# Optimization experiments

Hardware: AMD Instinct MI355X
Metric: run time of the kernel (lower is better)

The kernel has to match this reference:

```python
import jax, jax.numpy as jnp
import numpy as np

LORA_ALPHA = 2.0

def setup_inputs() -> dict:
    key = jax.random.key(0)
    k1, k2, k3, k4 = jax.random.split(key, 4)
    B, S, D_IN, D_OUT, R = 4, 2048, 4096, 4096, 16
    x = jax.random.normal(k1, (B, S, D_IN), dtype=jnp.float32)
    weight = jax.random.normal(k2, (D_OUT, D_IN), dtype=jnp.float32) * (1.0 / np.sqrt(D_IN))
    lora_A = jax.random.normal(k3, (R, D_IN), dtype=jnp.float32) * (1.0 / np.sqrt(D_IN))
    lora_B = jax.random.normal(k4, (D_OUT, R), dtype=jnp.float32) * 0.02
    return {"x": x, "weight": weight, "lora_A": lora_A, "lora_B": lora_B}

def reference(x, weight, lora_A, lora_B):
    # main_out = F.linear(x, weight) = x @ weight.T
    main_out = jnp.einsum('bsd,od->bso', x, weight)
    # Faithful to source: materialize lora_weight = B @ A (out x in), then full linear
    lora_weight = lora_B @ lora_A  # [out, in]
    lora_out = jnp.einsum('bsd,od->bso', x, lora_weight) * LORA_ALPHA
    return main_out + lora_out
```

## Files before the change

kernel.cpp:

```cpp
#include <hip/hip_runtime.h>
#include <stdint.h>

typedef __attribute__((ext_vector_type(8))) short bf16x8;
typedef __attribute__((ext_vector_type(4))) float f32x4;

#define GM 8192
#define GN 4096
#define GK 4096
#define KTILES (GK / 64)

__device__ __forceinline__ unsigned short f2bf(float f) {
  union { float f; unsigned int u; } c; c.f = f;
  unsigned int u = c.u;
  unsigned int r = u + 0x7FFFu + ((u >> 16) & 1u);
  return (unsigned short)(r >> 16);
}

__global__ __launch_bounds__(256) void cvt_x_kernel(const float* __restrict__ x,
                                                    unsigned short* __restrict__ xb) {
  int i = blockIdx.x * 256 + threadIdx.x;
  const float4* p = (const float4*)x + (size_t)i * 2;
  float4 a = p[0], b = p[1];
  unsigned short t[8] = { f2bf(a.x), f2bf(a.y), f2bf(a.z), f2bf(a.w),
                          f2bf(b.x), f2bf(b.y), f2bf(b.z), f2bf(b.w) };
  int4 pk; __builtin_memcpy(&pk, t, 16);
  ((int4*)xb)[i] = pk;
}

__global__ __launch_bounds__(256) void weff_kernel(const float* __restrict__ w,
                                                   const float* __restrict__ lA,
                                                   const float* __restrict__ lB,
                                                   unsigned short* __restrict__ wb) {
  const int K = GK;
  int idx = blockIdx.x * 256 + threadIdx.x;
  int o  = idx >> 9;
  int i0 = (idx & 511) << 3;

  float bl[16];
#pragma unroll
  for (int r = 0; r < 16; r += 4) {
    float4 v = *(const float4*)(lB + o * 16 + r);
    bl[r] = v.x; bl[r + 1] = v.y; bl[r + 2] = v.z; bl[r + 3] = v.w;
  }

  float acc[8] = {0.f, 0.f, 0.f, 0.f, 0.f, 0.f, 0.f, 0.f};
#pragma unroll
  for (int r = 0; r < 16; ++r) {
    float4 a0 = *(const float4*)(lA + (size_t)r * K + i0);
    float4 a1 = *(const float4*)(lA + (size_t)r * K + i0 + 4);
    acc[0] += bl[r] * a0.x; acc[1] += bl[r] * a0.y;
    acc[2] += bl[r] * a0.z; acc[3] += bl[r] * a0.w;
    acc[4] += bl[r] * a1.x; acc[5] += bl[r] * a1.y;
    acc[6] += bl[r] * a1.z; acc[7] += bl[r] * a1.w;
  }

  float4 w0 = *(const float4*)(w + (size_t)o * K + i0);
  float4 w1 = *(const float4*)(w + (size_t)o * K + i0 + 4);
  unsigned short t[8] = {
    f2bf(w0.x + 2.0f * acc[0]), f2bf(w0.y + 2.0f * acc[1]),
    f2bf(w0.z + 2.0f * acc[2]), f2bf(w0.w + 2.0f * acc[3]),
    f2bf(w1.x + 2.0f * acc[4]), f2bf(w1.y + 2.0f * acc[5]),
    f2bf(w1.z + 2.0f * acc[6]), f2bf(w1.w + 2.0f * acc[7]) };
  int4 pk; __builtin_memcpy(&pk, t, 16);
  ((int4*)wb)[idx] = pk;
}


__device__ __forceinline__ void gload16(const unsigned short* g, char* l) {
  __builtin_amdgcn_global_load_lds((__attribute__((address_space(1))) void*)g,
                                   (__attribute__((address_space(3))) void*)l, 16, 0, 0);
}

__device__ __forceinline__ void barrier_fence() {
  __builtin_amdgcn_sched_barrier(0);
  asm volatile("" ::: "memory");
  __builtin_amdgcn_s_barrier();
  asm volatile("" ::: "memory");
  __builtin_amdgcn_sched_barrier(0);
}

#define MFMA_BF16(a, b, c) __builtin_amdgcn_mfma_f32_16x16x32_bf16((a), (b), (c), 0, 0, 0)

template <int HALF>
__device__ __forceinline__ void stage_half(const unsigned short* A, const unsigned short* B,
                                           char* smem, int bm0, int bn0, int w, int lane,
                                           int kt, int buf) {
  int sr, isB;
  if constexpr (HALF == 0)      { sr = w + (w & 4);                 isB = 0; }
  else if constexpr (HALF == 1) { sr = ((w >> 1) << 2) + (w & 1);   isB = 1; }
  else if constexpr (HALF == 2) { sr = ((w >> 1) << 2) + (w & 1) + 2; isB = 1; }
  else                          { sr = w + (w & 4) + 4;             isB = 0; }
  const unsigned short* mat = isB ? B : A;
  const int grow = (isB ? bn0 : bm0) + sr * 16 + (lane >> 2);
  const int gcol = ((lane & 3) * 8) ^ ((lane & 32) ? 16 : 0);
#pragma unroll
  for (int sc = 0; sc < 2; ++sc) {
    const unsigned short* src = mat + (size_t)grow * GK + kt * 64 + sc * 32 + gcol;
    char* dst = smem + (buf << 16) + (isB ? 32768 : 0) + ((sr * 2 + sc) << 10);
    gload16(src, dst);
  }
}

__device__ __forceinline__ bf16x8 ldsA(const char* smem, int buf, int sr, int sc, int foff) {
  return *(const bf16x8*)(smem + (buf << 16) + ((sr * 2 + sc) << 10) + foff);
}
__device__ __forceinline__ bf16x8 ldsB(const char* smem, int buf, int sr, int sc, int foff) {
  return *(const bf16x8*)(smem + (buf << 16) + 32768 + ((sr * 2 + sc) << 10) + foff);
}

__global__ __launch_bounds__(512, 2) void gemm_bt_kernel(const unsigned short* __restrict__ A,
                                                         const unsigned short* __restrict__ B,
                                                         float* __restrict__ C) {
  __shared__ alignas(16) char smem[131072];

  const int t = threadIdx.x, lane = t & 63, w = t >> 6;
  const int wm = w >> 2, wn = w & 3;

  const int bid = blockIdx.x;
  const int wg  = (bid & 7) * (512 / 8) + (bid >> 3);
  const int bx = wg & 15, by = wg >> 4;
  const int bm0 = by * 256, bn0 = bx * 256;

  int foff = (lane & 15) * 64 + ((lane >> 4) << 4);
  foff ^= ((foff >> 9) & 1) << 5;

  stage_half<0>(A, B, smem, bm0, bn0, w, lane, 0, 0);
  stage_half<1>(A, B, smem, bm0, bn0, w, lane, 0, 0);
  stage_half<2>(A, B, smem, bm0, bn0, w, lane, 0, 0);
  stage_half<3>(A, B, smem, bm0, bn0, w, lane, 0, 0);
  asm volatile("s_waitcnt vmcnt(0)" ::: "memory");
  barrier_fence();

  f32x4 acc[8][4] = {};
  bf16x8 av[4][2], bv0[2][2], bv1[2][2];

  for (int kt = 0; kt < KTILES; ++kt) {
    const int cur = kt & 1, nxt = cur ^ 1;
    const bool last = (kt == KTILES - 1);

#pragma unroll
    for (int mi = 0; mi < 4; ++mi) {
      av[mi][0] = ldsA(smem, cur, wm * 8 + mi, 0, foff);
      av[mi][1] = ldsA(smem, cur, wm * 8 + mi, 1, foff);
    }
#pragma unroll
    for (int ni = 0; ni < 2; ++ni) {
      bv0[ni][0] = ldsB(smem, cur, wn * 4 + ni, 0, foff);
      bv0[ni][1] = ldsB(smem, cur, wn * 4 + ni, 1, foff);
    }
    if (!last) {
      stage_half<0>(A, B, smem, bm0, bn0, w, lane, kt + 1, nxt);
      asm volatile("s_waitcnt vmcnt(4)" ::: "memory");
    } else {
      asm volatile("s_waitcnt vmcnt(2)" ::: "memory");
    }
    barrier_fence();
    __builtin_amdgcn_s_setprio(1);
#pragma unroll
    for (int mi = 0; mi < 4; ++mi)
#pragma unroll
      for (int ni = 0; ni < 2; ++ni) {
        acc[mi][ni] = MFMA_BF16(av[mi][0], bv0[ni][0], acc[mi][ni]);
        acc[mi][ni] = MFMA_BF16(av[mi][1], bv0[ni][1], acc[mi][ni]);
      }
    __builtin_amdgcn_s_setprio(0);
    barrier_fence();

#pragma unroll
    for (int ni = 0; ni < 2; ++ni) {
      bv1[ni][0] = ldsB(smem, cur, wn * 4 + 2 + ni, 0, foff);
      bv1[ni][1] = ldsB(smem, cur, wn * 4 + 2 + ni, 1, foff);
    }
    if (!last) {
      stage_half<1>(A, B, smem, bm0, bn0, w, lane, kt + 1, nxt);
      asm volatile("s_waitcnt vmcnt(4)" ::: "memory");
    } else {
      asm volatile("s_waitcnt vmcnt(0)" ::: "memory");
    }
    barrier_fence();
    __builtin_amdgcn_s_setprio(1);
#pragma unroll
    for (int mi = 0; mi < 4; ++mi)
#pragma unroll
      for (int ni = 0; ni < 2; ++ni) {
        acc[mi][2 + ni] = MFMA_BF16(av[mi][0], bv1[ni][0], acc[mi][2 + ni]);
        acc[mi][2 + ni] = MFMA_BF16(av[mi][1], bv1[ni][1], acc[mi][2 + ni]);
      }
    __builtin_amdgcn_s_setprio(0);
    barrier_fence();

#pragma unroll
    for (int mi = 0; mi < 4; ++mi) {
      av[mi][0] = ldsA(smem, cur, wm * 8 + 4 + mi, 0, foff);
      av[mi][1] = ldsA(smem, cur, wm * 8 + 4 + mi, 1, foff);
    }
    if (!last) stage_half<2>(A, B, smem, bm0, bn0, w, lane, kt + 1, nxt);
    barrier_fence();
    __builtin_amdgcn_s_setprio(1);
#pragma unroll
    for (int mi = 0; mi < 4; ++mi)
#pragma unroll
      for (int ni = 0; ni < 2; ++ni) {
        acc[4 + mi][2 + ni] = MFMA_BF16(av[mi][0], bv1[ni][0], acc[4 + mi][2 + ni]);
        acc[4 + mi][2 + ni] = MFMA_BF16(av[mi][1], bv1[ni][1], acc[4 + mi][2 + ni]);
      }
    __builtin_amdgcn_s_setprio(0);
    barrier_fence();

    if (!last) {
      stage_half<3>(A, B, smem, bm0, bn0, w, lane, kt + 1, nxt);
      asm volatile("s_waitcnt vmcnt(4)" ::: "memory");
    }
    barrier_fence();
    __builtin_amdgcn_s_setprio(1);
#pragma unroll
    for (int mi = 0; mi < 4; ++mi)
#pragma unroll
      for (int ni = 0; ni < 2; ++ni) {
        acc[4 + mi][ni] = MFMA_BF16(av[mi][0], bv0[ni][0], acc[4 + mi][ni]);
        acc[4 + mi][ni] = MFMA_BF16(av[mi][1], bv0[ni][1], acc[4 + mi][ni]);
      }
    __builtin_amdgcn_s_setprio(0);
    barrier_fence();
  }

  const int orow = (lane >> 4) << 2;
#pragma unroll
  for (int mi = 0; mi < 8; ++mi) {
#pragma unroll
    for (int ni = 0; ni < 4; ++ni) {
      float* cp = C + (size_t)(bm0 + wm * 128 + mi * 16 + orow) * GN
                    + (bn0 + wn * 64 + ni * 16 + (lane & 15));
#pragma unroll
      for (int r = 0; r < 4; ++r)
        cp[(size_t)r * GN] = acc[mi][ni][r];
    }
  }
}

extern "C" void kernel_launch(void* const* d_in, const int* in_sizes, int n_in,
                              void* d_out, int out_size, void* d_ws, size_t ws_size,
                              hipStream_t stream) {
  const float* x  = (const float*)d_in[0];
  const float* w  = (const float*)d_in[1];
  const float* lA = (const float*)d_in[2];
  const float* lB = (const float*)d_in[3];
  float* out = (float*)d_out;

  const int M = GM, N = GN, K = GK;

  unsigned short* xb = (unsigned short*)d_ws;
  unsigned short* wb = xb + (size_t)M * K;

  cvt_x_kernel<<<dim3((M * K / 8) / 256), dim3(256), 0, stream>>>(x, xb);
  weff_kernel<<<dim3((N * K / 8) / 256), dim3(256), 0, stream>>>(w, lA, lB, wb);
  gemm_bt_kernel<<<dim3((M / 256) * (N / 256)), dim3(512), 0, stream>>>(xb, wb, out);
}
```

Measured before the change: 329.2 us.

## Deepen GEMM prefetch pipeline, drop sched barriers, and tile weff over 8 rows

The GEMM main loop now issues the first quarter of the K-tile two steps ahead into the current buffer, shifting every staging call earlier by one phase. The waitcnt thresholds are adjusted so more global loads stay in flight across barriers. The sched_barrier fences are removed in favour of plain barriers plus explicit lgkmcnt waits, which gives the compiler more freedom to interleave LDS reads with MFMAs. The weff kernel now computes an 8x8 output tile per thread so lora_A loads are reused across 8 rows, at the cost of more registers and scalar lora_B loads. The deeper prefetch risks LDS races if the buffer reuse ordering is wrong.

```diff
diff --git a/kernel.cpp b/kernel.cpp
--- a/kernel.cpp
+++ b/kernel.cpp
@@ -33,36 +33,42 @@
                                                    unsigned short* __restrict__ wb) {
   const int K = GK;
   int idx = blockIdx.x * 256 + threadIdx.x;
-  int o  = idx >> 9;
-  int i0 = (idx & 511) << 3;
-
-  float bl[16];
-#pragma unroll
-  for (int r = 0; r < 16; r += 4) {
-    float4 v = *(const float4*)(lB + o * 16 + r);
-    bl[r] = v.x; bl[r + 1] = v.y; bl[r + 2] = v.z; bl[r + 3] = v.w;
-  }
-
-  float acc[8] = {0.f, 0.f, 0.f, 0.f, 0.f, 0.f, 0.f, 0.f};
+  int cg = idx & 511;
+  int rg = idx >> 9;
+  int i0 = cg << 3;
+  int o0 = rg << 3;
+
+  float acc[8][8];
+#pragma unroll
+  for (int r = 0; r < 8; ++r)
+#pragma unroll
+    for (int c = 0; c < 8; ++c) acc[r][c] = 0.f;
+
 #pragma unroll
   for (int r = 0; r < 16; ++r) {
     float4 a0 = *(const float4*)(lA + (size_t)r * K + i0);
     float4 a1 = *(const float4*)(lA + (size_t)r * K + i0 + 4);
-    acc[0] += bl[r] * a0.x; acc[1] += bl[r] * a0.y;
-    acc[2] += bl[r] * a0.z; acc[3] += bl[r] * a0.w;
-    acc[4] += bl[r] * a1.x; acc[5] += bl[r] * a1.y;
-    acc[6] += bl[r] * a1.z; acc[7] += bl[r] * a1.w;
-  }
-
-  float4 w0 = *(const float4*)(w + (size_t)o * K + i0);
-  float4 w1 = *(const float4*)(w + (size_t)o * K + i0 + 4);
-  unsigned short t[8] = {
-    f2bf(w0.x + 2.0f * acc[0]), f2bf(w0.y + 2.0f * acc[1]),
-    f2bf(w0.z + 2.0f * acc[2]), f2bf(w0.w + 2.0f * acc[3]),
-    f2bf(w1.x + 2.0f * acc[4]), f2bf(w1.y + 2.0f * acc[5]),
-    f2bf(w1.z + 2.0f * acc[6]), f2bf(w1.w + 2.0f * acc[7]) };
-  int4 pk; __builtin_memcpy(&pk, t, 16);
-  ((int4*)wb)[idx] = pk;
+    float av[8] = { a0.x, a0.y, a0.z, a0.w, a1.x, a1.y, a1.z, a1.w };
+#pragma unroll
+    for (int row = 0; row < 8; ++row) {
+      float b = lB[(size_t)(o0 + row) * 16 + r];
+#pragma unroll
+      for (int c = 0; c < 8; ++c) acc[row][c] += b * av[c];
+    }
+  }
+
+#pragma unroll
+  for (int row = 0; row < 8; ++row) {
+    float4 w0 = *(const float4*)(w + (size_t)(o0 + row) * K + i0);
+    float4 w1 = *(const float4*)(w + (size_t)(o0 + row) * K + i0 + 4);
+    unsigned short t[8] = {
+      f2bf(w0.x + 2.0f * acc[row][0]), f2bf(w0.y + 2.0f * acc[row][1]),
+      f2bf(w0.z + 2.0f * acc[row][2]), f2bf(w0.w + 2.0f * acc[row][3]),
+      f2bf(w1.x + 2.0f * acc[row][4]), f2bf(w1.y + 2.0f * acc[row][5]),
+      f2bf(w1.z + 2.0f * acc[row][6]), f2bf(w1.w + 2.0f * acc[row][7]) };
+    int4 pk; __builtin_memcpy(&pk, t, 16);
+    *(int4*)(wb + (size_t)(o0 + row) * K + i0) = pk;
+  }
 }
 
 
@@ -71,12 +77,10 @@
                                    (__attribute__((address_space(3))) void*)l, 16, 0, 0);
 }
 
-__device__ __forceinline__ void barrier_fence() {
-  __builtin_amdgcn_sched_barrier(0);
+__device__ __forceinline__ void bar() {
   asm volatile("" ::: "memory");
   __builtin_amdgcn_s_barrier();
   asm volatile("" ::: "memory");
-  __builtin_amdgcn_sched_barrier(0);
 }
 
 #define MFMA_BF16(a, b, c) __builtin_amdgcn_mfma_f32_16x16x32_bf16((a), (b), (c), 0, 0, 0)
@@ -86,10 +90,10 @@
                                            char* smem, int bm0, int bn0, int w, int lane,
                                            int kt, int buf) {
   int sr, isB;
-  if constexpr (HALF == 0)      { sr = w + (w & 4);                 isB = 0; }
-  else if constexpr (HALF == 1) { sr = ((w >> 1) << 2) + (w & 1);   isB = 1; }
+  if constexpr (HALF == 0)      { sr = w + (w & 4);                   isB = 0; }
+  else if constexpr (HALF == 1) { sr = ((w >> 1) << 2) + (w & 1);     isB = 1; }
   else if constexpr (HALF == 2) { sr = ((w >> 1) << 2) + (w & 1) + 2; isB = 1; }
-  else                          { sr = w + (w & 4) + 4;             isB = 0; }
+  else                          { sr = w + (w & 4) + 4;               isB = 0; }
   const unsigned short* mat = isB ? B : A;
   const int grow = (isB ? bn0 : bm0) + sr * 16 + (lane >> 2);
   const int gcol = ((lane & 3) * 8) ^ ((lane & 32) ? 16 : 0);
@@ -128,15 +132,17 @@
   stage_half<1>(A, B, smem, bm0, bn0, w, lane, 0, 0);
   stage_half<2>(A, B, smem, bm0, bn0, w, lane, 0, 0);
   stage_half<3>(A, B, smem, bm0, bn0, w, lane, 0, 0);
-  asm volatile("s_waitcnt vmcnt(0)" ::: "memory");
-  barrier_fence();
+  stage_half<0>(A, B, smem, bm0, bn0, w, lane, 1, 1);
+  asm volatile("s_waitcnt vmcnt(6)" ::: "memory");
+  bar();
 
   f32x4 acc[8][4] = {};
   bf16x8 av[4][2], bv0[2][2], bv1[2][2];
 
   for (int kt = 0; kt < KTILES; ++kt) {
-    const int cur = kt & 1, nxt = cur ^ 1;
-    const bool last = (kt == KTILES - 1);
+    const int cur = kt & 1;
+    const bool n1 = (kt + 1 < KTILES);
+    const bool n2 = (kt + 2 < KTILES);
 
 #pragma unroll
     for (int mi = 0; mi < 4; ++mi) {
@@ -148,13 +154,14 @@
       bv0[ni][0] = ldsB(smem, cur, wn * 4 + ni, 0, foff);
       bv0[ni][1] = ldsB(smem, cur, wn * 4 + ni, 1, foff);
     }
-    if (!last) {
-      stage_half<0>(A, B, smem, bm0, bn0, w, lane, kt + 1, nxt);
-      asm volatile("s_waitcnt vmcnt(4)" ::: "memory");
+    if (n1) {
+      stage_half<1>(A, B, smem, bm0, bn0, w, lane, kt + 1, cur ^ 1);
+      asm volatile("s_waitcnt vmcnt(6)" ::: "memory");
     } else {
       asm volatile("s_waitcnt vmcnt(2)" ::: "memory");
     }
-    barrier_fence();
+    bar();
+    asm volatile("s_waitcnt lgkmcnt(0)" ::: "memory");
     __builtin_amdgcn_s_setprio(1);
 #pragma unroll
     for (int mi = 0; mi < 4; ++mi)
@@ -164,20 +171,21 @@
         acc[mi][ni] = MFMA_BF16(av[mi][1], bv0[ni][1], acc[mi][ni]);
       }
     __builtin_amdgcn_s_setprio(0);
-    barrier_fence();
+    bar();
 
 #pragma unroll
     for (int ni = 0; ni < 2; ++ni) {
       bv1[ni][0] = ldsB(smem, cur, wn * 4 + 2 + ni, 0, foff);
       bv1[ni][1] = ldsB(smem, cur, wn * 4 + 2 + ni, 1, foff);
     }
-    if (!last) {
-      stage_half<1>(A, B, smem, bm0, bn0, w, lane, kt + 1, nxt);
-      asm volatile("s_waitcnt vmcnt(4)" ::: "memory");
+    if (n1) {
+      stage_half<2>(A, B, smem, bm0, bn0, w, lane, kt + 1, cur ^ 1);
+      asm volatile("s_waitcnt vmcnt(6)" ::: "memory");
     } else {
       asm volatile("s_waitcnt vmcnt(0)" ::: "memory");
     }
-    barrier_fence();
+    bar();
+    asm volatile("s_waitcnt lgkmcnt(0)" ::: "memory");
     __builtin_amdgcn_s_setprio(1);
 #pragma unroll
     for (int mi = 0; mi < 4; ++mi)
@@ -187,15 +195,16 @@
         acc[mi][2 + ni] = MFMA_BF16(av[mi][1], bv1[ni][1], acc[mi][2 + ni]);
       }
     __builtin_amdgcn_s_setprio(0);
-    barrier_fence();
+    bar();
 
 #pragma unroll
     for (int mi = 0; mi < 4; ++mi) {
       av[mi][0] = ldsA(smem, cur, wm * 8 + 4 + mi, 0, foff);
       av[mi][1] = ldsA(smem, cur, wm * 8 + 4 + mi, 1, foff);
     }
-    if (!last) stage_half<2>(A, B, smem, bm0, bn0, w, lane, kt + 1, nxt);
-    barrier_fence();
+    if (n1) stage_half<3>(A, B, smem, bm0, bn0, w, lane, kt + 1, cur ^ 1);
+    bar();
+    asm volatile("s_waitcnt lgkmcnt(0)" ::: "memory");
     __builtin_amdgcn_s_setprio(1);
 #pragma unroll
     for (int mi = 0; mi < 4; ++mi)
@@ -205,13 +214,14 @@
         acc[4 + mi][2 + ni] = MFMA_BF16(av[mi][1], bv1[ni][1], acc[4 + mi][2 + ni]);
       }
     __builtin_amdgcn_s_setprio(0);
-    barrier_fence();
-
-    if (!last) {
-      stage_half<3>(A, B, smem, bm0, bn0, w, lane, kt + 1, nxt);
-      asm volatile("s_waitcnt vmcnt(4)" ::: "memory");
-    }
-    barrier_fence();
+    bar();
+
+    if (n2) stage_half<0>(A, B, smem, bm0, bn0, w, lane, kt + 2, cur);
+    if (n1) {
+      if (n2) asm volatile("s_waitcnt vmcnt(6)" ::: "memory");
+      else    asm volatile("s_waitcnt vmcnt(4)" ::: "memory");
+    }
+    bar();
     __builtin_amdgcn_s_setprio(1);
 #pragma unroll
     for (int mi = 0; mi < 4; ++mi)
@@ -221,7 +231,7 @@
         acc[4 + mi][ni] = MFMA_BF16(av[mi][1], bv0[ni][1], acc[4 + mi][ni]);
       }
     __builtin_amdgcn_s_setprio(0);
-    barrier_fence();
+    bar();
   }
 
   const int orow = (lane >> 4) << 2;
@@ -253,6 +263,6 @@
   unsigned short* wb = xb + (size_t)M * K;
 
   cvt_x_kernel<<<dim3((M * K / 8) / 256), dim3(256), 0, stream>>>(x, xb);
-  weff_kernel<<<dim3((N * K / 8) / 256), dim3(256), 0, stream>>>(w, lA, lB, wb);
+  weff_kernel<<<dim3((N / 8) * (K / 8) / 256), dim3(256), 0, stream>>>(w, lA, lB, wb);
   gemm_bt_kernel<<<dim3((M / 256) * (N / 256)), dim3(512), 0, stream>>>(xb, wb, out);
 }
```

Result: faster. 293.5 us (median of 4 runs) (-10.9%).
